# Kernel tuning notes

Measured on AMD Instinct MI355X. Metric: run time of the kernel, lower is better.

## Reference

```python
import jax, jax.numpy as jnp
import numpy as np

B, N, L, E, D = 16, 16384, 192, 128, 128


def setup_inputs() -> dict:
    key = jax.random.key(0)
    ks = jax.random.split(key, 16)
    s = 0.05
    return {
        "x_L_flattened": jax.random.normal(ks[0], (B, N), jnp.float32),
        "x_y_mask_flattened": jax.random.randint(ks[1], (B, N), 0, 2).astype(jnp.float32),
        "y_mask_L_flattened": jnp.zeros((B, N), jnp.float32),
        "x_y_mark": jax.random.normal(ks[2], (B, L, 1), jnp.float32),
        "variable_indices_flattened": jax.random.randint(ks[3], (B, N), 0, E),
        "time_indices_flattened": jax.random.randint(ks[4], (B, N), 0, L),
        "N_OBSERVATIONS_MAX": N,
        # learned params (stored [in, out]; torch Linear uses x @ W.T + b)
        "W_obs": jax.random.normal(ks[5], (2, D), jnp.float32) * s,
        "b_obs": jnp.zeros((D,), jnp.float32),
        "W_time": jax.random.normal(ks[6], (1, D), jnp.float32) * s,
        "b_time": jnp.zeros((D,), jnp.float32),
        "var_hyperedge_w": jax.random.normal(ks[7], (E, D), jnp.float32),
        "W_q": jax.random.normal(ks[8], (D, D), jnp.float32) * s,
        "b_q": jnp.zeros((D,), jnp.float32),
        "W_k": jax.random.normal(ks[9], (D, D), jnp.float32) * s,
        "b_k": jnp.zeros((D,), jnp.float32),
        "W_v": jax.random.normal(ks[10], (D, D), jnp.float32) * s,
        "b_v": jnp.zeros((D,), jnp.float32),
        "threshold": jnp.float32(0.5),
        "merge_coef": jnp.float32(0.5),
    }


def reference(x_L_flattened, x_y_mask_flattened, y_mask_L_flattened, x_y_mark,
              variable_indices_flattened, time_indices_flattened, N_OBSERVATIONS_MAX,
              W_obs, b_obs, W_time, b_time, var_hyperedge_w,
              W_q, b_q, W_k, b_k, W_v, b_v, threshold, merge_coef):
    mask = x_y_mask_flattened  # [B, N]
    # node features: value + (1 - mask + y_mask) channel -> [B, N, 2]
    feats = jnp.stack([x_L_flattened, 1.0 - mask + y_mask_L_flattened], axis=-1)
    # temporal incidence: node n belongs to time-edge l iff time_idx[n] == l; [B, L, N]
    ti = (time_indices_flattened[:, None, :] == jnp.arange(L)[None, :, None]).astype(jnp.float32)
    ti = ti * mask[:, None, :]
    # variable incidence: node n belongs to var-edge e iff var_idx[n] == e; [B, E, N]
    vi = (jnp.arange(E)[None, :, None] == variable_indices_flattened[:, None, :]).astype(jnp.float32)
    vi = vi * mask[:, None, :]
    # encoders
    obs = jax.nn.relu(feats @ W_obs + b_obs) * mask[..., None]          # [B, N, D]
    temp_he = jnp.sin(x_y_mark @ W_time + b_time)                        # [B, L, D]
    var_he = jax.nn.relu(jnp.broadcast_to(var_hyperedge_w, (B, E, D)))   # [B, E, D]
    # IrregularityAwareAttention over variable hyperedges with incidence as aux
    q = var_he @ W_q + b_q
    k = var_he @ W_k + b_k
    v = var_he @ W_v + b_v
    att = jnp.einsum('bed,bfd->bef', q, k) / (D ** 0.5)                  # [B, E, E]
    att_aux = jnp.einsum('ben,bfn->bef', vi, vi) / (N_OBSERVATIONS_MAX ** 0.5)
    merge = (att > threshold) & (att_aux != 0)
    att = jnp.where(merge, (1.0 - merge_coef) * att + merge_coef * att_aux, att)
    attn = jax.nn.softmax(att, axis=-1)
    out = jnp.einsum('bef,bfd->bed', attn, v)                            # [B, E, D]
    return (obs, temp_he, out, ti, vi)
```

## Files before the change

### kernel.cpp

```cpp
#include <hip/hip_runtime.h>

#define Bb 16
#define Nn 16384
#define Ll 192
#define Ee 128
#define Dd 128


#define QKV_NB   128
#define TEMP_NB  1536
#define FILL_NB  20480
#define OBS_NB   32768
#define TEMP_B0  (QKV_NB)
#define FILL_B0  (TEMP_B0 + TEMP_NB)
#define OBS_B0   (FILL_B0 + FILL_NB)
#define GRID1    (OBS_B0 + OBS_NB)

__global__ __launch_bounds__(256) void k_main(
    const float* __restrict__ var_w,
    const float* __restrict__ Wq, const float* __restrict__ bq,
    const float* __restrict__ Wk, const float* __restrict__ bk,
    const float* __restrict__ Wv, const float* __restrict__ bv,
    const float* __restrict__ x, const float* __restrict__ mask,
    const float* __restrict__ ymask,
    const float* __restrict__ W_obs, const float* __restrict__ b_obs,
    const float* __restrict__ mark, const float* __restrict__ Wt,
    const float* __restrict__ bt,
    float* __restrict__ zfill,
    float* __restrict__ q, float* __restrict__ kT, float* __restrict__ v,
    float* __restrict__ obs, float* __restrict__ temp)
{
    __shared__ float sh[Dd];
    const int tid = threadIdx.x;
    const unsigned bx = blockIdx.x;

    if (bx >= OBS_B0) {
        const int g   = (bx - OBS_B0) * 256 + tid;
        const int row = g >> 5;
        const int d   = (g & 31) << 2;

        const float m  = mask[row];
        const float xv = x[row];
        const float f1 = 1.0f - m + ymask[row];

        const float4 w0 = *reinterpret_cast<const float4*>(W_obs + d);
        const float4 w1 = *reinterpret_cast<const float4*>(W_obs + Dd + d);
        const float4 bb = *reinterpret_cast<const float4*>(b_obs + d);

        float4 o;
        o.x = fmaxf(fmaf(xv, w0.x, fmaf(f1, w1.x, bb.x)), 0.0f) * m;
        o.y = fmaxf(fmaf(xv, w0.y, fmaf(f1, w1.y, bb.y)), 0.0f) * m;
        o.z = fmaxf(fmaf(xv, w0.z, fmaf(f1, w1.z, bb.z)), 0.0f) * m;
        o.w = fmaxf(fmaf(xv, w0.w, fmaf(f1, w1.w, bb.w)), 0.0f) * m;
        *reinterpret_cast<float4*>(obs + ((size_t)row << 7) + d) = o;
    } else if (bx >= FILL_B0) {
        float4* p = reinterpret_cast<float4*>(zfill)
                  + ((size_t)(bx - FILL_B0) << 10) + tid;
        const float4 z = make_float4(0.0f, 0.0f, 0.0f, 0.0f);
        p[0]   = z;
        p[256] = z;
        p[512] = z;
        p[768] = z;
    } else if (bx >= TEMP_B0) {
        const int idx = (bx - TEMP_B0) * 256 + tid;
        const int d = idx & 127;
        const int r = idx >> 7;
        temp[idx] = sinf(fmaf(mark[r], Wt[d], bt[d]));
    } else {
        const int e = bx;
        if (tid < Dd) sh[tid] = fmaxf(var_w[e * Dd + tid], 0.0f);
        __syncthreads();
        if (tid < Dd) {
            float aq = bq[tid], ak = bk[tid], av = bv[tid];
            #pragma unroll 4
            for (int j = 0; j < Dd; ++j) {
                const float hj = sh[j];
                aq = fmaf(hj, Wq[j * Dd + tid], aq);
                ak = fmaf(hj, Wk[j * Dd + tid], ak);
                av = fmaf(hj, Wv[j * Dd + tid], av);
            }
            q[e * Dd + tid]  = aq;
            kT[tid * Dd + e] = ak;
            v[e * Dd + tid]  = av;
        }
    }
}

__global__ __launch_bounds__(256) void k_scatter(
    const int* __restrict__ tidx, const int* __restrict__ vidx,
    const float* __restrict__ mask,
    float* __restrict__ ti, float* __restrict__ vi,
    float* __restrict__ cnt_part)
{
    __shared__ float sh[Ee];
    const int tid = threadIdx.x;
    const int g  = blockIdx.x * 256 + tid;
    const int b  = g >> 12;
    const int n4 = (g & 4095) << 2;

    const int4   t4 = *reinterpret_cast<const int4*>(tidx + b * Nn + n4);
    const int4   v4 = *reinterpret_cast<const int4*>(vidx + b * Nn + n4);
    const float4 m4 = *reinterpret_cast<const float4*>(mask + b * Nn + n4);

    if (tid < Ee) sh[tid] = 0.0f;
    __syncthreads();

    float* tib = ti + (((size_t)b * Ll) << 14);
    float* vib = vi + (((size_t)b * Ee) << 14);

    if (m4.x != 0.0f) {
        atomicAdd(&sh[v4.x], 1.0f);
        tib[((size_t)t4.x << 14) + n4]     = m4.x;
        vib[((size_t)v4.x << 14) + n4]     = m4.x;
    }
    if (m4.y != 0.0f) {
        atomicAdd(&sh[v4.y], 1.0f);
        tib[((size_t)t4.y << 14) + n4 + 1] = m4.y;
        vib[((size_t)v4.y << 14) + n4 + 1] = m4.y;
    }
    if (m4.z != 0.0f) {
        atomicAdd(&sh[v4.z], 1.0f);
        tib[((size_t)t4.z << 14) + n4 + 2] = m4.z;
        vib[((size_t)v4.z << 14) + n4 + 2] = m4.z;
    }
    if (m4.w != 0.0f) {
        atomicAdd(&sh[v4.w], 1.0f);
        tib[((size_t)t4.w << 14) + n4 + 3] = m4.w;
        vib[((size_t)v4.w << 14) + n4 + 3] = m4.w;
    }

    __syncthreads();
    if (tid < Ee) cnt_part[blockIdx.x * Ee + tid] = sh[tid];
}

__global__ __launch_bounds__(128) void k_soft(
    const float* __restrict__ q, const float* __restrict__ kT,
    const float* __restrict__ v, const float* __restrict__ cnt_part,
    const float* __restrict__ thr_p, const float* __restrict__ mc_p,
    const int* __restrict__ nobs_p, float* __restrict__ outp)
{
    __shared__ float qr[Dd];
    __shared__ float attn[Ee];
    __shared__ float red[5];
    const int b = blockIdx.x >> 7;
    const int e = blockIdx.x & 127;
    const int f = threadIdx.x;

    qr[f] = q[e * Dd + f];

    float cp = (f < 16) ? cnt_part[(b * 16 + f) * Ee + e] : 0.0f;
    #pragma unroll
    for (int off = 8; off > 0; off >>= 1) cp += __shfl_xor(cp, off);
    if (f == 0) red[4] = cp;
    __syncthreads();

    float acc0 = 0.0f;
    #pragma unroll 4
    for (int d = 0; d < Dd; ++d) acc0 = fmaf(qr[d], kT[d * Dd + f], acc0);
    float a = acc0 * 0.08838834764831845f;

    if (f == e) {
        const float c = red[4];
        const float thr = *thr_p;
        if (c != 0.0f && a > thr) {
            const float mc  = *mc_p;
            const float aux = c / sqrtf((float)(*nobs_p));
            a = (1.0f - mc) * a + mc * aux;
        }
    }

    float mx = a;
    #pragma unroll
    for (int off = 32; off > 0; off >>= 1) mx = fmaxf(mx, __shfl_xor(mx, off));
    if ((f & 63) == 0) red[f >> 6] = mx;
    __syncthreads();
    mx = fmaxf(red[0], red[1]);

    const float ex = expf(a - mx);
    float s = ex;
    #pragma unroll
    for (int off = 32; off > 0; off >>= 1) s += __shfl_xor(s, off);
    if ((f & 63) == 0) red[2 + (f >> 6)] = s;
    __syncthreads();
    s = red[2] + red[3];

    attn[f] = ex / s;
    __syncthreads();

    const int d = f;
    float acc = 0.0f;
    #pragma unroll 4
    for (int j = 0; j < Ee; ++j) acc = fmaf(attn[j], v[j * Dd + d], acc);
    outp[((size_t)(b * Ee + e) << 7) + d] = acc;
}

extern "C" void kernel_launch(void* const* d_in, const int* in_sizes, int n_in,
                              void* d_out, int out_size, void* d_ws, size_t ws_size,
                              hipStream_t stream) {
    (void)in_sizes; (void)n_in; (void)out_size; (void)ws_size;

    const float* x      = (const float*)d_in[0];
    const float* mask   = (const float*)d_in[1];
    const float* ymask  = (const float*)d_in[2];
    const float* mark   = (const float*)d_in[3];
    const int*   vidx   = (const int*)d_in[4];
    const int*   tidx   = (const int*)d_in[5];
    const int*   nobs   = (const int*)d_in[6];
    const float* W_obs  = (const float*)d_in[7];
    const float* b_obs  = (const float*)d_in[8];
    const float* W_time = (const float*)d_in[9];
    const float* b_time = (const float*)d_in[10];
    const float* var_w  = (const float*)d_in[11];
    const float* W_q    = (const float*)d_in[12];
    const float* b_q    = (const float*)d_in[13];
    const float* W_k    = (const float*)d_in[14];
    const float* b_k    = (const float*)d_in[15];
    const float* W_v    = (const float*)d_in[16];
    const float* b_v    = (const float*)d_in[17];
    const float* thr    = (const float*)d_in[18];
    const float* mc     = (const float*)d_in[19];

    float* out_base = (float*)d_out;
    float* obs  = out_base;
    float* temp = out_base + 33554432;
    float* attO = out_base + 33947648;
    float* ti   = out_base + 34209792;
    float* vi   = out_base + 84541440;

    float* ws       = (float*)d_ws;
    float* cnt_part = ws;
    float* q        = ws + 32768;
    float* kT       = ws + 49152;
    float* v        = ws + 65536;

    k_main<<<GRID1, 256, 0, stream>>>(var_w,
                                      W_q, b_q, W_k, b_k, W_v, b_v,
                                      x, mask, ymask, W_obs, b_obs,
                                      mark, W_time, b_time,
                                      ti ,
                                      q, kT, v, obs, temp);
    k_scatter<<<256, 256, 0, stream>>>(tidx, vidx, mask, ti, vi, cnt_part);
    k_soft<<<Bb * Ee, Dd, 0, stream>>>(q, kT, v, cnt_part, thr, mc, nobs, attO);
}
```

Measured before the change: 552.4 us.

## Use grid-stride loops with nontemporal stores in the fused fill kernel

```diff
diff --git a/kernel.cpp b/kernel.cpp
--- a/kernel.cpp
+++ b/kernel.cpp
@@ -8,13 +8,19 @@
 
 
 #define QKV_NB   128
-#define TEMP_NB  1536
-#define FILL_NB  20480
-#define OBS_NB   32768
+#define TEMP_NB  512
+#define FILL_NB  2048
+#define OBS_NB   2048
 #define TEMP_B0  (QKV_NB)
 #define FILL_B0  (TEMP_B0 + TEMP_NB)
 #define OBS_B0   (FILL_B0 + FILL_NB)
 #define GRID1    (OBS_B0 + OBS_NB)
+
+#define FILL_LANES (FILL_NB * 256)
+#define OBS_LANES  (OBS_NB * 256)
+#define TEMP_LANES (TEMP_NB * 256)
+
+using f4 = __attribute__((ext_vector_type(4))) float;
 
 __global__ __launch_bounds__(256) void k_main(
     const float* __restrict__ var_w,
@@ -35,37 +41,47 @@
     const unsigned bx = blockIdx.x;
 
     if (bx >= OBS_B0) {
-        const int g   = (bx - OBS_B0) * 256 + tid;
-        const int row = g >> 5;
-        const int d   = (g & 31) << 2;
-
-        const float m  = mask[row];
-        const float xv = x[row];
-        const float f1 = 1.0f - m + ymask[row];
+        const unsigned lane = (bx - OBS_B0) * 256 + tid;
+        const int d = (lane & 31) << 2;
 
         const float4 w0 = *reinterpret_cast<const float4*>(W_obs + d);
         const float4 w1 = *reinterpret_cast<const float4*>(W_obs + Dd + d);
         const float4 bb = *reinterpret_cast<const float4*>(b_obs + d);
 
-        float4 o;
-        o.x = fmaxf(fmaf(xv, w0.x, fmaf(f1, w1.x, bb.x)), 0.0f) * m;
-        o.y = fmaxf(fmaf(xv, w0.y, fmaf(f1, w1.y, bb.y)), 0.0f) * m;
-        o.z = fmaxf(fmaf(xv, w0.z, fmaf(f1, w1.z, bb.z)), 0.0f) * m;
-        o.w = fmaxf(fmaf(xv, w0.w, fmaf(f1, w1.w, bb.w)), 0.0f) * m;
-        *reinterpret_cast<float4*>(obs + ((size_t)row << 7) + d) = o;
+        #pragma unroll 4
+        for (int i = 0; i < 16; ++i) {
+            const unsigned idx = lane + (unsigned)i * OBS_LANES;
+            const int row = idx >> 5;
+
+            const float m  = mask[row];
+            const float xv = x[row];
+            const float f1 = 1.0f - m + ymask[row];
+
+            f4 o;
+            o.x = fmaxf(fmaf(xv, w0.x, fmaf(f1, w1.x, bb.x)), 0.0f) * m;
+            o.y = fmaxf(fmaf(xv, w0.y, fmaf(f1, w1.y, bb.y)), 0.0f) * m;
+            o.z = fmaxf(fmaf(xv, w0.z, fmaf(f1, w1.z, bb.z)), 0.0f) * m;
+            o.w = fmaxf(fmaf(xv, w0.w, fmaf(f1, w1.w, bb.w)), 0.0f) * m;
+            __builtin_nontemporal_store(
+                o, reinterpret_cast<f4*>(obs + ((size_t)row << 7) + d));
+        }
     } else if (bx >= FILL_B0) {
-        float4* p = reinterpret_cast<float4*>(zfill)
-                  + ((size_t)(bx - FILL_B0) << 10) + tid;
-        const float4 z = make_float4(0.0f, 0.0f, 0.0f, 0.0f);
-        p[0]   = z;
-        p[256] = z;
-        p[512] = z;
-        p[768] = z;
+        f4* p = reinterpret_cast<f4*>(zfill);
+        const size_t lane = (size_t)(bx - FILL_B0) * 256 + tid;
+        const f4 z = {0.0f, 0.0f, 0.0f, 0.0f};
+        #pragma unroll 8
+        for (int i = 0; i < 40; ++i)
+            __builtin_nontemporal_store(z, p + lane + (size_t)i * FILL_LANES);
     } else if (bx >= TEMP_B0) {
-        const int idx = (bx - TEMP_B0) * 256 + tid;
-        const int d = idx & 127;
-        const int r = idx >> 7;
-        temp[idx] = sinf(fmaf(mark[r], Wt[d], bt[d]));
+        const int lane = (bx - TEMP_B0) * 256 + tid;
+        #pragma unroll
+        for (int i = 0; i < 3; ++i) {
+            const int idx = lane + i * TEMP_LANES;
+            const int d = idx & 127;
+            const int r = idx >> 7;
+            __builtin_nontemporal_store(sinf(fmaf(mark[r], Wt[d], bt[d])),
+                                        temp + idx);
+        }
     } else {
         const int e = bx;
         if (tid < Dd) sh[tid] = fmaxf(var_w[e * Dd + tid], 0.0f);
```

After: 579.7 us. 1.05x slower.
